# Performance work log

Measured on AMD Instinct MI355X. Metric: run time of the kernel, lower is better.

## Reference

```python
import jax, jax.numpy as jnp
import numpy as np

H = 64  # hidden size == embed dim

def _lstm_scan(xp, w_hh):
    # xp: [T, B, 4H] precomputed input projections (+ both biases)
    # PyTorch gate order: i, f, g, o
    B = xp.shape[1]
    h0 = jnp.zeros((B, H), xp.dtype)
    c0 = jnp.zeros((B, H), xp.dtype)
    def step(carry, xt):
        h, c = carry
        g = xt + h @ w_hh.T
        i = jax.nn.sigmoid(g[:, 0*H:1*H])
        f = jax.nn.sigmoid(g[:, 1*H:2*H])
        gc = jnp.tanh(g[:, 2*H:3*H])
        o = jax.nn.sigmoid(g[:, 3*H:4*H])
        c = f * c + i * gc
        h = o * jnp.tanh(c)
        return (h, c), h
    _, hs = jax.lax.scan(step, (h0, c0), xp)
    return hs  # [T, B, H]


def setup_inputs() -> dict:
    key = jax.random.key(0)
    ks = jax.random.split(key, 12)
    B, T, V, C = 256, 2000, 2000, 12
    s_ih = 1.0 / np.sqrt(H)
    def u(k, shape):
        return jax.random.uniform(k, shape, jnp.float32, -s_ih, s_ih)
    return {
        "x": jax.random.randint(ks[0], (B, T), 0, V, dtype=jnp.int32),
        "emb": jax.random.normal(ks[1], (V, H), jnp.float32),
        "w_ih_f": u(ks[2], (4 * H, H)),
        "w_hh_f": u(ks[3], (4 * H, H)),
        "b_ih_f": u(ks[4], (4 * H,)),
        "b_hh_f": u(ks[5], (4 * H,)),
        "w_ih_b": u(ks[6], (4 * H, H)),
        "w_hh_b": u(ks[7], (4 * H, H)),
        "b_ih_b": u(ks[8], (4 * H,)),
        "b_hh_b": u(ks[9], (4 * H,)),
        "w_fc": u(ks[10], (C, 2 * H)),
        "b_fc": u(ks[11], (C,)),
    }


def reference(x, emb, w_ih_f, w_hh_f, b_ih_f, b_hh_f, w_ih_b, w_hh_b, b_ih_b, b_hh_b, w_fc, b_fc):
    # embedding with padding_idx=0 (row 0 is zero)
    table = emb.at[0].set(0.0)
    e = table[x]                                   # [B, T, H]
    # precompute input projections once (batched GEMM), fold both biases
    xp_f = jnp.einsum('bth,gh->btg', e, w_ih_f) + b_ih_f + b_hh_f
    xp_b = jnp.einsum('bth,gh->btg', e, w_ih_b) + b_ih_b + b_hh_b
    hs_f = _lstm_scan(jnp.swapaxes(xp_f, 0, 1), w_hh_f)            # [T, B, H]
    hs_b = _lstm_scan(jnp.swapaxes(xp_b, 0, 1)[::-1], w_hh_b)      # [T, B, H], reversed time
    # output at original last timestep: fwd last scan step, bwd first scan step
    y_last = jnp.concatenate([hs_f[-1], hs_b[0]], axis=-1)         # [B, 2H]
    return y_last @ w_fc.T + b_fc                                  # [B, 12]
```

## Files before the change

### kernel.cpp

```cpp
#include <hip/hip_runtime.h>

#define H  64
#define G4 256

typedef float vf4 __attribute__((ext_vector_type(4)));

__device__ __forceinline__ float sigm(float x) {
    return __builtin_amdgcn_rcpf(1.0f + __expf(-x));
}
__device__ __forceinline__ float tanh_s(float x) {
    return fmaf(2.0f, sigm(2.0f * x), -1.0f);
}

__device__ __forceinline__ float bcast(float v, int lane) {
    return __int_as_float(__builtin_amdgcn_readlane(__float_as_int(v), lane));
}

__global__ __launch_bounds__(256)
void proj_kernel(const float* __restrict__ emb,
                 const float* __restrict__ w_ih,
                 const float* __restrict__ b_ih,
                 const float* __restrict__ b_hh,
                 float* __restrict__ P,
                 int V)
{
    const int j  = threadIdx.x;
    const int v0 = blockIdx.x * 8;

    __shared__ float es[8][H];
    {
        int idx = j;
        #pragma unroll
        for (int rep = 0; rep < 2; ++rep, idx += 256) {
            int r = idx >> 6, col = idx & 63;
            int v = v0 + r;
            float val = 0.0f;
            if (v < V && v != 0) val = emb[v * H + col];
            es[r][col] = val;
        }
    }

    vf4 w[16];
    const vf4* w4 = reinterpret_cast<const vf4*>(w_ih + j * H);
    #pragma unroll
    for (int i = 0; i < 16; ++i) w[i] = w4[i];

    float bias = b_ih[j] + b_hh[j];
    __syncthreads();

    #pragma unroll
    for (int r = 0; r < 8; ++r) {
        int v = v0 + r;
        if (v >= V) break;
        float a0 = 0, a1 = 0, a2 = 0, a3 = 0;
        #pragma unroll
        for (int i = 0; i < 16; ++i) {
            a0 = fmaf(es[r][4*i+0], w[i][0], a0);
            a1 = fmaf(es[r][4*i+1], w[i][1], a1);
            a2 = fmaf(es[r][4*i+2], w[i][2], a2);
            a3 = fmaf(es[r][4*i+3], w[i][3], a3);
        }
        P[v * G4 + j] = bias + ((a0 + a1) + (a2 + a3));
    }
}

__global__ __launch_bounds__(256, 1)
void lstm_kernel(const int* __restrict__ x,
                 const float* __restrict__ Pf,
                 const float* __restrict__ w_hh,
                 const float* __restrict__ w_ih_b,
                 const float* __restrict__ b_ih_b,
                 const float* __restrict__ b_hh_b,
                 const float* __restrict__ emb,
                 const float* __restrict__ w_fc,
                 const float* __restrict__ b_fc,
                 float* __restrict__ out,
                 int T)
{
    const int b    = blockIdx.x;
    const int j    = threadIdx.x;
    const int lane = j & 63;
    const int gate = j >> 6;

    const vf4* w4 = reinterpret_cast<const vf4*>(w_hh + j * H);
    vf4 q0  = w4[0],  q1  = w4[1],  q2  = w4[2],  q3  = w4[3];
    vf4 q4  = w4[4],  q5  = w4[5],  q6  = w4[6],  q7  = w4[7];
    vf4 q8  = w4[8],  q9  = w4[9],  q10 = w4[10], q11 = w4[11];
    vf4 q12 = w4[12], q13 = w4[13], q14 = w4[14], q15 = w4[15];
    asm volatile("" : "+v"(q0),  "+v"(q1),  "+v"(q2),  "+v"(q3));
    asm volatile("" : "+v"(q4),  "+v"(q5),  "+v"(q6),  "+v"(q7));
    asm volatile("" : "+v"(q8),  "+v"(q9),  "+v"(q10), "+v"(q11));
    asm volatile("" : "+v"(q12), "+v"(q13), "+v"(q14), "+v"(q15));

    const float ms = (gate == 2) ? 2.0f : 1.0f;
    const float Aa = (gate == 2) ? 2.0f : 1.0f;
    const float Ba = (gate == 2) ? -1.0f : 0.0f;

    __shared__ vf4  g_t[2][64];
    __shared__ float hf_s[H];
    __shared__ float hb_s[H];
    __shared__ float e_s[H];

    const int* __restrict__ xrow = x + (long)b * T;

    float h = 0.0f;
    float c = 0.0f;

    int   tok_next = (T > 1) ? xrow[1] : 0;
    float p_cur    = Pf[xrow[0] * G4 + j];

    float* gslot = reinterpret_cast<float*>(g_t) + (lane * 4 + gate);

    for (int t = 0; t < T; ++t) {
        float p_next  = Pf[tok_next * G4 + j];
        int tok_next2 = (t + 2 < T) ? xrow[t + 2] : 0;

        float a0 = 0, a1 = 0, a2 = 0, a3 = 0;
        #define KSTEP(Q, base) { \
            float h0 = bcast(h, base+0); \
            float h1 = bcast(h, base+1); \
            float h2 = bcast(h, base+2); \
            float h3 = bcast(h, base+3); \
            a0 = fmaf(Q[0], h0, a0); \
            a1 = fmaf(Q[1], h1, a1); \
            a2 = fmaf(Q[2], h2, a2); \
            a3 = fmaf(Q[3], h3, a3); }
        KSTEP(q0,   0) KSTEP(q1,   4) KSTEP(q2,   8) KSTEP(q3,  12)
        KSTEP(q4,  16) KSTEP(q5,  20) KSTEP(q6,  24) KSTEP(q7,  28)
        KSTEP(q8,  32) KSTEP(q9,  36) KSTEP(q10, 40) KSTEP(q11, 44)
        KSTEP(q12, 48) KSTEP(q13, 52) KSTEP(q14, 56) KSTEP(q15, 60)
        #undef KSTEP

        float s   = p_cur + ((a0 + a1) + (a2 + a3));
        float act = fmaf(Aa, sigm(ms * s), Ba);

        const int ph = t & 1;
        gslot[ph << 8] = act;
        asm volatile("s_waitcnt lgkmcnt(0)" ::: "memory");
        __builtin_amdgcn_s_barrier();

        vf4 gv = g_t[ph][lane];
        c = fmaf(gv[1], c, gv[0] * gv[2]);
        h = gv[3] * tanh_s(c);

        p_cur    = p_next;
        tok_next = tok_next2;
    }

    int tokL = xrow[T - 1];
    if (gate == 0) hf_s[lane] = h;
    if (j < H) e_s[j] = (tokL != 0) ? emb[tokL * H + j] : 0.0f;
    __syncthreads();

    float accb = 0.0f;
    {
        const vf4* wb4 = reinterpret_cast<const vf4*>(w_ih_b + j * H);
        #pragma unroll
        for (int i = 0; i < 16; ++i) {
            vf4 wq = wb4[i];
            accb = fmaf(wq[0], e_s[4*i+0], accb);
            accb = fmaf(wq[1], e_s[4*i+1], accb);
            accb = fmaf(wq[2], e_s[4*i+2], accb);
            accb = fmaf(wq[3], e_s[4*i+3], accb);
        }
    }
    float gb = accb + b_ih_b[j] + b_hh_b[j];
    gslot[0] = fmaf(Aa, sigm(ms * gb), Ba);
    __syncthreads();

    if (j < H) {
        vf4 gv = g_t[0][j];
        float cb = gv[0] * gv[2];
        hb_s[j] = gv[3] * tanh_s(cb);
    }
    __syncthreads();

    if (j < 12) {
        float acc = b_fc[j];
        const float* wf = w_fc + j * (2 * H);
        #pragma unroll
        for (int k = 0; k < H; ++k) acc = fmaf(hf_s[k], wf[k], acc);
        #pragma unroll
        for (int k = 0; k < H; ++k) acc = fmaf(hb_s[k], wf[H + k], acc);
        out[b * 12 + j] = acc;
    }
}

extern "C" void kernel_launch(void* const* d_in, const int* in_sizes, int n_in,
                              void* d_out, int out_size, void* d_ws, size_t ws_size,
                              hipStream_t stream)
{
    const int*   x      = (const int*)  d_in[0];
    const float* emb    = (const float*)d_in[1];
    const float* w_ih_f = (const float*)d_in[2];
    const float* w_hh_f = (const float*)d_in[3];
    const float* b_ih_f = (const float*)d_in[4];
    const float* b_hh_f = (const float*)d_in[5];
    const float* w_ih_b = (const float*)d_in[6];
    const float* b_ih_b = (const float*)d_in[8];
    const float* b_hh_b = (const float*)d_in[9];
    const float* w_fc   = (const float*)d_in[10];
    const float* b_fc   = (const float*)d_in[11];
    float* out = (float*)d_out;

    const int B = out_size / 12;
    const int T = in_sizes[0] / B;
    const int V = in_sizes[1] / H;

    float* Pf = (float*)d_ws;

    int pblocks = (V + 7) / 8;
    proj_kernel<<<pblocks, 256, 0, stream>>>(emb, w_ih_f, b_ih_f, b_hh_f, Pf, V);
    lstm_kernel<<<B, 256, 0, stream>>>(x, Pf, w_hh_f, w_ih_b, b_ih_b, b_hh_b,
                                       emb, w_fc, b_fc, out, T);
}
```

Before: 959.2 us.

## Split LSTM recurrent matvec across K-quarters with 512 threads and LDS reduction

The recurrent kernel grows from 256 to 512 threads per block. Each wave now handles a quarter of the hidden dimension for two gate rows, so the serial dot-product chain per thread drops from 64 FMAs to 16. Partial sums go to a swizzled LDS buffer, and every lane reduces the four partials for all four gates of its hidden unit. The gate nonlinearities and the cell update are computed redundantly in each wave. The projection table is re-laid out gate-interleaved so each lane loads its four gate inputs as one vector. This trades more LDS traffic, a wider barrier and duplicated activations for a shorter per-step critical path.

New measurement: 1.351 ms. 40.8% more time.

```diff
diff --git a/kernel.cpp b/kernel.cpp
--- a/kernel.cpp
+++ b/kernel.cpp
@@ -48,6 +48,7 @@
     float bias = b_ih[j] + b_hh[j];
     __syncthreads();
 
+    const int slot = (j & 63) * 4 + (j >> 6);
     #pragma unroll
     for (int r = 0; r < 8; ++r) {
         int v = v0 + r;
@@ -60,13 +61,13 @@
             a2 = fmaf(es[r][4*i+2], w[i][2], a2);
             a3 = fmaf(es[r][4*i+3], w[i][3], a3);
         }
-        P[v * G4 + j] = bias + ((a0 + a1) + (a2 + a3));
-    }
-}
-
-__global__ __launch_bounds__(256, 1)
+        P[v * G4 + slot] = bias + ((a0 + a1) + (a2 + a3));
+    }
+}
+
+__global__ __launch_bounds__(512, 2)
 void lstm_kernel(const int* __restrict__ x,
-                 const float* __restrict__ Pf,
+                 const float* __restrict__ P2,
                  const float* __restrict__ w_hh,
                  const float* __restrict__ w_ih_b,
                  const float* __restrict__ b_ih_b,
@@ -78,83 +79,95 @@
                  int T)
 {
     const int b    = blockIdx.x;
-    const int j    = threadIdx.x;
-    const int lane = j & 63;
-    const int gate = j >> 6;
-
-    const vf4* w4 = reinterpret_cast<const vf4*>(w_hh + j * H);
-    vf4 q0  = w4[0],  q1  = w4[1],  q2  = w4[2],  q3  = w4[3];
-    vf4 q4  = w4[4],  q5  = w4[5],  q6  = w4[6],  q7  = w4[7];
-    vf4 q8  = w4[8],  q9  = w4[9],  q10 = w4[10], q11 = w4[11];
-    vf4 q12 = w4[12], q13 = w4[13], q14 = w4[14], q15 = w4[15];
-    asm volatile("" : "+v"(q0),  "+v"(q1),  "+v"(q2),  "+v"(q3));
-    asm volatile("" : "+v"(q4),  "+v"(q5),  "+v"(q6),  "+v"(q7));
-    asm volatile("" : "+v"(q8),  "+v"(q9),  "+v"(q10), "+v"(q11));
-    asm volatile("" : "+v"(q12), "+v"(q13), "+v"(q14), "+v"(q15));
-
-    const float ms = (gate == 2) ? 2.0f : 1.0f;
-    const float Aa = (gate == 2) ? 2.0f : 1.0f;
-    const float Ba = (gate == 2) ? -1.0f : 0.0f;
-
-    __shared__ vf4  g_t[2][64];
+    const int tid  = threadIdx.x;
+    const int lane = tid & 63;
+    const int wv   = tid >> 6;
+    const int kq   = wv & 3;
+    const int rg   = wv >> 2;
+
+    const int r0 = rg * 128 + lane;
+    const int r1 = r0 + 64;
+
+    vf4 w0[4], w1[4];
+    {
+        const vf4* a = reinterpret_cast<const vf4*>(w_hh + r0 * H + kq * 16);
+        const vf4* c4 = reinterpret_cast<const vf4*>(w_hh + r1 * H + kq * 16);
+        #pragma unroll
+        for (int i = 0; i < 4; ++i) { w0[i] = a[i]; w1[i] = c4[i]; }
+    }
+
+    __shared__ float pl[2][256][4];
     __shared__ float hf_s[H];
     __shared__ float hb_s[H];
     __shared__ float e_s[H];
 
     const int* __restrict__ xrow = x + (long)b * T;
+    const float* __restrict__ Pme = P2 + lane * 4;
 
     float h = 0.0f;
     float c = 0.0f;
 
-    int   tok_next = (T > 1) ? xrow[1] : 0;
-    float p_cur    = Pf[xrow[0] * G4 + j];
-
-    float* gslot = reinterpret_cast<float*>(g_t) + (lane * 4 + gate);
+    int tok_next = (T > 1) ? xrow[1] : 0;
+    vf4 p_cur = *reinterpret_cast<const vf4*>(Pme + (size_t)xrow[0] * G4);
+
+    const int s = kq ^ ((lane >> 4) & 3);
+    float* wr0 = &pl[0][r0][s];
+    float* wr1 = &pl[0][r1][s];
+    const int kb = kq * 16;
 
     for (int t = 0; t < T; ++t) {
-        float p_next  = Pf[tok_next * G4 + j];
+        vf4 p_next = *reinterpret_cast<const vf4*>(Pme + (size_t)tok_next * G4);
         int tok_next2 = (t + 2 < T) ? xrow[t + 2] : 0;
 
-        float a0 = 0, a1 = 0, a2 = 0, a3 = 0;
-        #define KSTEP(Q, base) { \
-            float h0 = bcast(h, base+0); \
-            float h1 = bcast(h, base+1); \
-            float h2 = bcast(h, base+2); \
-            float h3 = bcast(h, base+3); \
-            a0 = fmaf(Q[0], h0, a0); \
-            a1 = fmaf(Q[1], h1, a1); \
-            a2 = fmaf(Q[2], h2, a2); \
-            a3 = fmaf(Q[3], h3, a3); }
-        KSTEP(q0,   0) KSTEP(q1,   4) KSTEP(q2,   8) KSTEP(q3,  12)
-        KSTEP(q4,  16) KSTEP(q5,  20) KSTEP(q6,  24) KSTEP(q7,  28)
-        KSTEP(q8,  32) KSTEP(q9,  36) KSTEP(q10, 40) KSTEP(q11, 44)
-        KSTEP(q12, 48) KSTEP(q13, 52) KSTEP(q14, 56) KSTEP(q15, 60)
-        #undef KSTEP
-
-        float s   = p_cur + ((a0 + a1) + (a2 + a3));
-        float act = fmaf(Aa, sigm(ms * s), Ba);
+        float a00 = 0, a01 = 0, a10 = 0, a11 = 0;
+        #pragma unroll
+        for (int m = 0; m < 16; m += 2) {
+            float hb0 = bcast(h, kb + m);
+            float hb1 = bcast(h, kb + m + 1);
+            a00 = fmaf(w0[m >> 2][m & 3], hb0, a00);
+            a10 = fmaf(w1[m >> 2][m & 3], hb0, a10);
+            a01 = fmaf(w0[(m + 1) >> 2][(m + 1) & 3], hb1, a01);
+            a11 = fmaf(w1[(m + 1) >> 2][(m + 1) & 3], hb1, a11);
+        }
+        float part0 = a00 + a01;
+        float part1 = a10 + a11;
 
         const int ph = t & 1;
-        gslot[ph << 8] = act;
+        wr0[ph * 1024] = part0;
+        wr1[ph * 1024] = part1;
         asm volatile("s_waitcnt lgkmcnt(0)" ::: "memory");
         __builtin_amdgcn_s_barrier();
 
-        vf4 gv = g_t[ph][lane];
-        c = fmaf(gv[1], c, gv[0] * gv[2]);
-        h = gv[3] * tanh_s(c);
+        const vf4* pb = reinterpret_cast<const vf4*>(pl[ph]);
+        vf4 qi = pb[lane];
+        vf4 qf = pb[64 + lane];
+        vf4 qg = pb[128 + lane];
+        vf4 qo = pb[192 + lane];
+        float si = ((qi[0] + qi[1]) + (qi[2] + qi[3])) + p_cur[0];
+        float sf = ((qf[0] + qf[1]) + (qf[2] + qf[3])) + p_cur[1];
+        float sg = ((qg[0] + qg[1]) + (qg[2] + qg[3])) + p_cur[2];
+        float so = ((qo[0] + qo[1]) + (qo[2] + qo[3])) + p_cur[3];
+
+        float i_ = sigm(si);
+        float f_ = sigm(sf);
+        float g_ = tanh_s(sg);
+        float o_ = sigm(so);
+        c = fmaf(f_, c, i_ * g_);
+        h = o_ * tanh_s(c);
 
         p_cur    = p_next;
         tok_next = tok_next2;
     }
 
     int tokL = xrow[T - 1];
-    if (gate == 0) hf_s[lane] = h;
-    if (j < H) e_s[j] = (tokL != 0) ? emb[tokL * H + j] : 0.0f;
-    __syncthreads();
-
-    float accb = 0.0f;
-    {
-        const vf4* wb4 = reinterpret_cast<const vf4*>(w_ih_b + j * H);
+    if (wv == 0) hf_s[lane] = h;
+    if (tid < H) e_s[tid] = (tokL != 0) ? emb[tokL * H + tid] : 0.0f;
+    __syncthreads();
+
+    float* gb_s = reinterpret_cast<float*>(pl);
+    if (tid < 256) {
+        float accb = 0.0f;
+        const vf4* wb4 = reinterpret_cast<const vf4*>(w_ih_b + tid * H);
         #pragma unroll
         for (int i = 0; i < 16; ++i) {
             vf4 wq = wb4[i];
@@ -163,26 +176,28 @@
             accb = fmaf(wq[2], e_s[4*i+2], accb);
             accb = fmaf(wq[3], e_s[4*i+3], accb);
         }
-    }
-    float gb = accb + b_ih_b[j] + b_hh_b[j];
-    gslot[0] = fmaf(Aa, sigm(ms * gb), Ba);
-    __syncthreads();
-
-    if (j < H) {
-        vf4 gv = g_t[0][j];
-        float cb = gv[0] * gv[2];
-        hb_s[j] = gv[3] * tanh_s(cb);
-    }
-    __syncthreads();
-
-    if (j < 12) {
-        float acc = b_fc[j];
-        const float* wf = w_fc + j * (2 * H);
+        float gb = accb + b_ih_b[tid] + b_hh_b[tid];
+        gb_s[tid] = ((tid >> 6) == 2) ? tanh_s(gb) : sigm(gb);
+    }
+    __syncthreads();
+
+    if (tid < H) {
+        float i_ = gb_s[tid];
+        float gg = gb_s[2*H + tid];
+        float go = gb_s[3*H + tid];
+        float cb = i_ * gg;
+        hb_s[tid] = go * tanh_s(cb);
+    }
+    __syncthreads();
+
+    if (tid < 12) {
+        float acc = b_fc[tid];
+        const float* wf = w_fc + tid * (2 * H);
         #pragma unroll
         for (int k = 0; k < H; ++k) acc = fmaf(hf_s[k], wf[k], acc);
         #pragma unroll
         for (int k = 0; k < H; ++k) acc = fmaf(hb_s[k], wf[H + k], acc);
-        out[b * 12 + j] = acc;
+        out[b * 12 + tid] = acc;
     }
 }
 
@@ -211,6 +226,6 @@
 
     int pblocks = (V + 7) / 8;
     proj_kernel<<<pblocks, 256, 0, stream>>>(emb, w_ih_f, b_ih_f, b_hh_f, Pf, V);
-    lstm_kernel<<<B, 256, 0, stream>>>(x, Pf, w_hh_f, w_ih_b, b_ih_b, b_hh_b,
+    lstm_kernel<<<B, 512, 0, stream>>>(x, Pf, w_hh_f, w_ih_b, b_ih_b, b_hh_b,
                                        emb, w_fc, b_fc, out, T);
 }
```
